# Kernel tuning notes

Hardware: AMD Instinct MI355X
Metric: run time of the kernel (lower is better)

Reference implementation:

```python
import jax, jax.numpy as jnp
import numpy as np

B = 32
HIST, C, H, W = 10, 11, 15, 20
D, NH, NL = 256, 4, 4
HD = D // NH
OUT, ADIM = 256, 20
L = HIST * H * W + 1  # 3001 tokens incl. cls
VIS = HIST * C * H * W  # 33000


def layernorm(x, g, b, eps=1e-5):
    m = jnp.mean(x, axis=-1, keepdims=True)
    v = jnp.mean((x - m) ** 2, axis=-1, keepdims=True)
    return (x - m) * jax.lax.rsqrt(v + eps) * g + b


def rope_1d(x):
    # x: [B, NH, L, HD]
    l, hd = x.shape[2], x.shape[3]
    t = jnp.arange(l, dtype=x.dtype)
    freqs = 10000.0 ** (-jnp.arange(0, hd, 2, dtype=x.dtype) / hd)
    emb = t[:, None] * freqs[None, :]            # [L, HD/2]
    emb = jnp.concatenate([emb, emb], axis=-1)   # [L, HD]
    cos = jnp.cos(emb)[None, None]
    sin = jnp.sin(emb)[None, None]
    x1, x2 = x[..., : hd // 2], x[..., hd // 2 :]
    rot = jnp.concatenate([-x2, x1], axis=-1)
    return x * cos + rot * sin


def lightning_attn(x, qw, kw, vw, ow, gq, bq, gk, bk):
    b, l, _ = x.shape
    q = layernorm(x @ qw, gq, bq)
    k = layernorm(x @ kw, gk, bk)
    v = x @ vw
    split = lambda a: a.reshape(b, l, NH, HD).transpose(0, 2, 1, 3)  # [B,NH,L,HD]
    q, k, v = split(q), split(k), split(v)
    q = jax.nn.silu(rope_1d(q))
    k = jax.nn.silu(rope_1d(k))
    kv = jnp.einsum('bhld,bhle->bhde', k, v)            # O(L) kv accumulation
    out = jnp.einsum('bhld,bhde->bhle', q, kv)
    out = out / jnp.sqrt(jnp.asarray(HD, x.dtype))
    out = out.transpose(0, 2, 1, 3).reshape(b, l, D)
    return out @ ow


def forward(obs_stack, proj_w, proj_b, cls_token, qw, kw, vw, ow, gq, bq, gk, bk,
            n1g, n1b, n2g, n2b, w1, b1, w2, b2, fng, fnb, out_w, out_b):
    b = obs_stack.shape[0]
    obs_feat = obs_stack[:, :VIS]
    action_feat = obs_stack[:, VIS:]
    vision = obs_feat.reshape(b, HIST, C, H, W).transpose(0, 1, 3, 4, 2)  # [B,T,H,W,C]
    x = vision @ proj_w + proj_b                                          # [B,T,H,W,D]
    x = x.reshape(b, -1, D)
    cls = jnp.broadcast_to(cls_token, (b, 1, D))
    x = jnp.concatenate([cls, x], axis=1)                                 # [B,L,D]
    for i in range(NL):
        h = lightning_attn(layernorm(x, n1g[i], n1b[i]), qw[i], kw[i], vw[i], ow[i],
                           gq[i], bq[i], gk[i], bk[i])
        x = x + h
        y = layernorm(x, n2g[i], n2b[i])
        y = jax.nn.gelu(y @ w1[i] + b1[i], approximate=False) @ w2[i] + b2[i]
        x = x + y
    x = layernorm(x, fng, fnb)
    cls_out = x[:, 0, :]
    final = jnp.concatenate([cls_out, action_feat], axis=1)
    return final @ out_w + out_b


def setup_inputs() -> dict:
    key = jax.random.key(0)
    ks = jax.random.split(key, 16)
    s = 0.02
    n = lambda k, shp: jax.random.normal(k, shp, dtype=jnp.float32) * s
    inp = {
        'obs_stack': jax.random.normal(ks[0], (B, VIS + ADIM), dtype=jnp.float32),
        'proj_w': n(ks[1], (C, D)),
        'proj_b': jnp.zeros((D,), jnp.float32),
        'cls_token': jax.random.normal(ks[2], (1, 1, D), dtype=jnp.float32),
        'qw': n(ks[3], (NL, D, D)),
        'kw': n(ks[4], (NL, D, D)),
        'vw': n(ks[5], (NL, D, D)),
        'ow': n(ks[6], (NL, D, D)),
        'gq': jnp.ones((NL, D), jnp.float32),
        'bq': jnp.zeros((NL, D), jnp.float32),
        'gk': jnp.ones((NL, D), jnp.float32),
        'bk': jnp.zeros((NL, D), jnp.float32),
        'n1g': jnp.ones((NL, D), jnp.float32),
        'n1b': jnp.zeros((NL, D), jnp.float32),
        'n2g': jnp.ones((NL, D), jnp.float32),
        'n2b': jnp.zeros((NL, D), jnp.float32),
        'w1': n(ks[7], (NL, D, 4 * D)),
        'b1': jnp.zeros((NL, 4 * D), jnp.float32),
        'w2': n(ks[8], (NL, 4 * D, D)),
        'b2': jnp.zeros((NL, D), jnp.float32),
        'fng': jnp.ones((D,), jnp.float32),
        'fnb': jnp.zeros((D,), jnp.float32),
        'out_w': n(ks[9], (D + ADIM, OUT)),
        'out_b': jnp.zeros((OUT,), jnp.float32),
    }
    return inp


def reference(obs_stack, proj_w, proj_b, cls_token, qw, kw, vw, ow, gq, bq, gk, bk,
              n1g, n1b, n2g, n2b, w1, b1, w2, b2, fng, fnb, out_w, out_b):
    return forward(obs_stack, proj_w, proj_b, cls_token, qw, kw, vw, ow, gq, bq, gk, bk,
                   n1g, n1b, n2g, n2b, w1, b1, w2, b2, fng, fnb, out_w, out_b)
```

## Files before the change

kernel.cpp:

```cpp
#include <hip/hip_runtime.h>
#include <math.h>

typedef unsigned short u16;
typedef __attribute__((ext_vector_type(8))) short short8;
typedef __attribute__((ext_vector_type(4))) short short4v;
typedef __attribute__((ext_vector_type(4))) float f32x4;

constexpr int B_    = 32;
constexpr int HIST_ = 10, C_ = 11, H_ = 15, W_ = 20;
constexpr int D_    = 256, NH_ = 4, NL_ = 4, HD_ = 64;
constexpr int OUT_  = 256, ADIM_ = 20;
constexpr int L_    = HIST_*H_*W_ + 1;
constexpr int VIS_  = HIST_*C_*H_*W_;
constexpr int NTOK  = B_*L_;
constexpr int OBSROW = VIS_ + ADIM_;
constexpr int PADR  = 128;

__device__ __forceinline__ float bf2f(u16 u) {
    return __uint_as_float(((unsigned)u) << 16);
}
__device__ __forceinline__ u16 f2bf(float f) {
    unsigned u = __float_as_uint(f);
    u = u + 0x7FFFu + ((u >> 16) & 1u);
    return (u16)(u >> 16);
}
__device__ __forceinline__ f32x4 mfma16(short8 a, short8 b, f32x4 c) {
    return __builtin_amdgcn_mfma_f32_16x16x32_bf16(a, b, c, 0, 0, 0);
}
__device__ __forceinline__ void gload16(const u16* gsrc, u16* ldsdst) {
    __builtin_amdgcn_global_load_lds(
        (const __attribute__((address_space(1))) unsigned int*)gsrc,
        (__attribute__((address_space(3))) unsigned int*)ldsdst,
        16, 0, 0);
}
__device__ __forceinline__ float gelu_fast(float v) {
    float t2 = 1.5957691216f*(v + 0.044715f*v*v*v);
    return v / (1.f + __expf(-t2));
}

__global__ void zero_kernel(float* __restrict__ p, int n) {
    int i = blockIdx.x*256 + threadIdx.x;
    if (i < n) p[i] = 0.f;
}

__global__ void wcvt_kernel(const float* __restrict__ src, u16* __restrict__ dst,
                            int Nn, int Kk, int dstLS, int dstOff) {
    int idx = blockIdx.x*256 + threadIdx.x;
    int tot = NL_*Nn*Kk;
    if (idx >= tot) return;
    int l = idx / (Nn*Kk);
    int rem = idx % (Nn*Kk);
    int n = rem / Kk, k = rem % Kk;
    dst[(size_t)l*dstLS + (size_t)(dstOff+n)*Kk + k] = f2bf(src[(size_t)l*Kk*Nn + (size_t)k*Nn + n]);
}

__global__ void rope_table_kernel(float* __restrict__ tab) {
    int idx = blockIdx.x*256 + threadIdx.x;
    if (idx >= L_*32) return;
    int t = idx >> 5, i = idx & 31;
    float freq = powf(10000.f, -2.f*(float)i/(float)HD_);
    float ang = (float)t * freq;
    tab[idx*2]   = cosf(ang);
    tab[idx*2+1] = sinf(ang);
}

__global__ __launch_bounds__(256) void proj_kernel(const float* __restrict__ obs,
        const float* __restrict__ pw, const float* __restrict__ pb,
        const float* __restrict__ cls, u16* __restrict__ x) {
    int wave = threadIdx.x >> 6, lane = threadIdx.x & 63;
    int n = blockIdx.x*4 + wave;
    if (n >= NTOK) return;
    int b = n / L_, l = n % L_;
    float4 acc;
    if (l == 0) {
        acc = ((const float4*)cls)[lane];
    } else {
        int t = l - 1;
        int hist = t / (H_*W_);
        int rem  = t % (H_*W_);
        float vv = 0.f;
        if (lane < C_) vv = obs[(size_t)b*OBSROW + hist*(C_*H_*W_) + lane*(H_*W_) + rem];
        acc = ((const float4*)pb)[lane];
        #pragma unroll
        for (int c = 0; c < C_; ++c) {
            float vc = __shfl(vv, c);
            float4 w4 = ((const float4*)(pw + c*D_))[lane];
            acc.x += vc*w4.x; acc.y += vc*w4.y; acc.z += vc*w4.z; acc.w += vc*w4.w;
        }
    }
    short4v o;
    o.x = (short)f2bf(acc.x); o.y = (short)f2bf(acc.y);
    o.z = (short)f2bf(acc.z); o.w = (short)f2bf(acc.w);
    *(short4v*)(x + (size_t)n*D_ + lane*4) = o;
}

__global__ __launch_bounds__(256) void ln_f2b_kernel(const u16* __restrict__ in,
        const float* __restrict__ g, const float* __restrict__ bt,
        u16* __restrict__ out, int ntok) {
    int wave = threadIdx.x >> 6, lane = threadIdx.x & 63;
    int n = blockIdx.x*4 + wave;
    if (n >= ntok) return;
    short4v raw = *(const short4v*)(in + (size_t)n*D_ + lane*4);
    float v0 = bf2f((u16)raw.x), v1 = bf2f((u16)raw.y), v2 = bf2f((u16)raw.z), v3 = bf2f((u16)raw.w);
    float s  = v0+v1+v2+v3;
    float sq = v0*v0+v1*v1+v2*v2+v3*v3;
    #pragma unroll
    for (int off = 32; off; off >>= 1) { s += __shfl_xor(s, off); sq += __shfl_xor(sq, off); }
    float mean = s * (1.f/D_);
    float var  = sq * (1.f/D_) - mean*mean;
    float r = rsqrtf(var + 1e-5f);
    float4 gg = ((const float4*)g)[lane];
    float4 bb = ((const float4*)bt)[lane];
    short4v o;
    o.x = (short)f2bf((v0-mean)*r*gg.x + bb.x);
    o.y = (short)f2bf((v1-mean)*r*gg.y + bb.y);
    o.z = (short)f2bf((v2-mean)*r*gg.z + bb.z);
    o.w = (short)f2bf((v3-mean)*r*gg.w + bb.w);
    *(short4v*)(out + (size_t)n*D_ + lane*4) = o;
}

template<int EPI, bool PB>
__global__ __launch_bounds__(256) void gemm_bf16(const u16* __restrict__ A, int lda,
        const u16* __restrict__ Wt, const float* __restrict__ bias,
        u16* __restrict__ Cb, u16* __restrict__ Xres, int M, int N, int K, int ldc) {
    __shared__ u16 As[2*128*32];
    __shared__ u16 Bs[2*128*32];
    const int gx = gridDim.x;
    int n = blockIdx.y * gx + blockIdx.x;
    const int nwg = gx * gridDim.y;
    if ((nwg & 7) == 0) n = (n & 7) * (nwg >> 3) + (n >> 3);
    const int bx = n % gx, by = n / gx;
    const int row0 = by*128, col0 = bx*128;

    size_t zrow = 0;
    if (PB) {
        int z = blockIdx.z;
        A  += (size_t)z * M * lda;
        Wt += (size_t)z * N * K;
        zrow = (size_t)z * M;
    }

    const int tid = threadIdx.x;
    const int wid = tid >> 6, lane = tid & 63;
    const int wr = wid >> 1, wc = wid & 1;

    f32x4 acc[4][4];
    #pragma unroll
    for (int i = 0; i < 4; ++i)
        #pragma unroll
        for (int j = 0; j < 4; ++j) {
            f32x4 z; z.x = 0.f; z.y = 0.f; z.z = 0.f; z.w = 0.f;
            acc[i][j] = z;
        }

    const int r0s = wid*32 + (lane>>2);
    const int r1s = r0s + 16;
    const int s0 = ((lane&3) - (r0s>>1)) & 3;
    const int s1 = ((lane&3) - (r1s>>1)) & 3;
    const u16* a0p = A  + (size_t)(row0 + r0s)*lda + s0*8;
    const u16* a1p = A  + (size_t)(row0 + r1s)*lda + s1*8;
    const u16* b0p = Wt + (size_t)(col0 + r0s)*K + s0*8;
    const u16* b1p = Wt + (size_t)(col0 + r1s)*K + s1*8;
    u16* lA0 = As + (wid*2+0)*512;
    u16* lA1 = As + (wid*2+1)*512;
    u16* lB0 = Bs + (wid*2+0)*512;
    u16* lB1 = Bs + (wid*2+1)*512;

    const int kg = lane >> 4, li = lane & 15;
    int aoff[4], boff[4];
    #pragma unroll
    for (int mi = 0; mi < 4; ++mi) {
        int row = wr*64 + mi*16 + li;
        aoff[mi] = row*32 + ((kg + (row>>1)) & 3)*8;
    }
    #pragma unroll
    for (int ni = 0; ni < 4; ++ni) {
        int row = wc*64 + ni*16 + li;
        boff[ni] = row*32 + ((kg + (row>>1)) & 3)*8;
    }

    auto stage = [&](int k0) {
        #pragma unroll
        for (int t = 0; t < 2; ++t) {
            const int ko = k0 + t*32;
            const int lo = t*4096;
            gload16(a0p + ko, lA0 + lo); gload16(a1p + ko, lA1 + lo);
            gload16(b0p + ko, lB0 + lo); gload16(b1p + ko, lB1 + lo);
        }
    };

    stage(0);
    const int nk2 = K >> 6;
    for (int ks = 0; ks < nk2; ++ks) {
        __syncthreads();
        short8 af[2][4], bfr[2][4];
        #pragma unroll
        for (int t = 0; t < 2; ++t) {
            #pragma unroll
            for (int mi = 0; mi < 4; ++mi) af[t][mi] = *(const short8*)(As + t*4096 + aoff[mi]);
            #pragma unroll
            for (int ni = 0; ni < 4; ++ni) bfr[t][ni] = *(const short8*)(Bs + t*4096 + boff[ni]);
        }
        __syncthreads();
        if (ks + 1 < nk2) stage((ks + 1) << 6);
        #pragma unroll
        for (int t = 0; t < 2; ++t)
            #pragma unroll
            for (int mi = 0; mi < 4; ++mi)
                #pragma unroll
                for (int ni = 0; ni < 4; ++ni)
                    acc[mi][ni] = mfma16(af[t][mi], bfr[t][ni], acc[mi][ni]);
    }

    #pragma unroll
    for (int mi = 0; mi < 4; ++mi) {
        int rbase = row0 + wr*64 + mi*16 + kg*4;
        #pragma unroll
        for (int ni = 0; ni < 4; ++ni) {
            int col = col0 + wc*64 + ni*16 + li;
            #pragma unroll
            for (int r = 0; r < 4; ++r) {
                int row = rbase + r;
                if (row >= M) continue;
                float v = acc[mi][ni][r];
                if (EPI == 1 || EPI == 3 || EPI == 4) v += bias[col];
                if (EPI == 1) v = gelu_fast(v);
                if (EPI == 2 || EPI == 3) {
                    size_t xi = (zrow + row)*(size_t)ldc + col;
                    Xres[xi] = f2bf(bf2f(Xres[xi]) + v);
                } else {
                    Cb[(zrow + row)*(size_t)ldc + col] = f2bf(v);
                }
            }
        }
    }
}

template<int EPI, bool PB>
__global__ __launch_bounds__(512) void gemm_wide(const u16* __restrict__ A, int lda,
        const u16* __restrict__ Wt, const float* __restrict__ bias,
        u16* __restrict__ Cb, int M, int N, int K, int ldc,
        const float* __restrict__ gqv = nullptr, const float* __restrict__ bqv = nullptr,
        const float* __restrict__ gkv = nullptr, const float* __restrict__ bkv = nullptr,
        const float* __restrict__ tab = nullptr) {
    __shared__ u16 As[2*4096];
    __shared__ u16 Bs[2*8192];
    const int gx = gridDim.x;
    int n = blockIdx.y * gx + blockIdx.x;
    const int nwg = gx * gridDim.y;
    if ((nwg & 7) == 0) n = (n & 7) * (nwg >> 3) + (n >> 3);
    const int bx = n % gx, by = n / gx;
    const int row0 = by*128, col0 = bx*256;

    size_t zrow = 0;
    if (PB) {
        int z = blockIdx.z;
        A  += (size_t)z * M * lda;
        Wt += (size_t)z * N * K;
        zrow = (size_t)z * M;
    }

    const int tid = threadIdx.x;
    const int wid = tid >> 6, lane = tid & 63;
    const int kg = lane >> 4, li = lane & 15;

    f32x4 acc[16];
    #pragma unroll
    for (int i = 0; i < 16; ++i) { f32x4 z; z.x=0.f; z.y=0.f; z.z=0.f; z.w=0.f; acc[i]=z; }

    const int ra = wid*16 + (lane>>2);
    const int sa = ((lane&3) - (ra>>1)) & 3;
    const u16* agp = A + (size_t)(row0 + ra)*lda + sa*8;
    const int lAo = wid*512;
    const int rb0 = (wid*2+0)*16 + (lane>>2);
    const int rb1 = (wid*2+1)*16 + (lane>>2);
    const int sb0 = ((lane&3) - (rb0>>1)) & 3;
    const int sb1 = ((lane&3) - (rb1>>1)) & 3;
    const u16* bgp0 = Wt + (size_t)(col0 + rb0)*K + sb0*8;
    const u16* bgp1 = Wt + (size_t)(col0 + rb1)*K + sb1*8;
    const int lB0o = (wid*2+0)*512;
    const int lB1o = (wid*2+1)*512;

    const int arow = wid*16 + li;
    const int aoff = arow*32 + ((kg + (arow>>1)) & 3)*8;
    int boff[16];
    #pragma unroll
    for (int ni = 0; ni < 16; ++ni) {
        int row = ni*16 + li;
        boff[ni] = row*32 + ((kg + (row>>1)) & 3)*8;
    }

    auto stage = [&](int k0) {
        #pragma unroll
        for (int t = 0; t < 2; ++t) {
            const int ko = k0 + t*32;
            gload16(agp  + ko, As + t*4096 + lAo);
            gload16(bgp0 + ko, Bs + t*8192 + lB0o);
            gload16(bgp1 + ko, Bs + t*8192 + lB1o);
        }
    };

    stage(0);
    const int nk2 = K >> 6;
    for (int ks = 0; ks < nk2; ++ks) {
        __syncthreads();
        short8 af0 = *(const short8*)(As + aoff);
        short8 b0[8], b1[8];
        #pragma unroll
        for (int ni = 0; ni < 8; ++ni) b0[ni] = *(const short8*)(Bs + boff[ni]);
        #pragma unroll
        for (int ni = 0; ni < 8; ++ni) acc[ni] = mfma16(af0, b0[ni], acc[ni]);
        #pragma unroll
        for (int ni = 0; ni < 8; ++ni) b1[ni] = *(const short8*)(Bs + boff[8+ni]);
        #pragma unroll
        for (int ni = 0; ni < 8; ++ni) acc[8+ni] = mfma16(af0, b1[ni], acc[8+ni]);
        short8 af1 = *(const short8*)(As + 4096 + aoff);
        #pragma unroll
        for (int ni = 0; ni < 8; ++ni) b0[ni] = *(const short8*)(Bs + 8192 + boff[ni]);
        #pragma unroll
        for (int ni = 0; ni < 8; ++ni) b1[ni] = *(const short8*)(Bs + 8192 + boff[8+ni]);
        __syncthreads();
        if (ks + 1 < nk2) stage((ks + 1) << 6);
        #pragma unroll
        for (int ni = 0; ni < 8; ++ni) acc[ni]   = mfma16(af1, b0[ni], acc[ni]);
        #pragma unroll
        for (int ni = 0; ni < 8; ++ni) acc[8+ni] = mfma16(af1, b1[ni], acc[8+ni]);
    }

    if constexpr (EPI == 2 || EPI == 3) {
        const bool doLN = (EPI == 2) ? (bx < 2) : (bx == 0);
        const float* g  = (EPI == 2) ? (bx ? gkv : gqv) : gkv;
        const float* bt = (EPI == 2) ? (bx ? bkv : bqv) : bkv;
        #pragma unroll
        for (int r = 0; r < 4; ++r) {
            const int row = row0 + wid*16 + kg*4 + r;
            const bool ok = row < M;
            if (doLN) {
                float o[16];
                float s = 0.f, sq = 0.f;
                #pragma unroll
                for (int ni = 0; ni < 16; ++ni) { float v = acc[ni][r]; o[ni] = v; s += v; sq += v*v; }
                s += __shfl_xor(s, 1); sq += __shfl_xor(sq, 1);
                s += __shfl_xor(s, 2); sq += __shfl_xor(sq, 2);
                s += __shfl_xor(s, 4); sq += __shfl_xor(sq, 4);
                s += __shfl_xor(s, 8); sq += __shfl_xor(sq, 8);
                float mean = s * (1.f/256.f);
                float var  = sq * (1.f/256.f) - mean*mean;
                float rstd = rsqrtf(var + 1e-5f);
                #pragma unroll
                for (int ni = 0; ni < 16; ++ni) {
                    int col = ni*16 + li;
                    o[ni] = (o[ni] - mean)*rstd*g[col] + bt[col];
                }
                if (ok) {
                    int l = row % L_;
                    #pragma unroll
                    for (int ni = 0; ni < 16; ++ni) {
                        int i32 = (ni&1)*16 + li;
                        float cs = tab[((size_t)l*32 + i32)*2];
                        float sn = tab[((size_t)l*32 + i32)*2 + 1];
                        float prt = o[ni^2];
                        float rv = ((ni&3) < 2) ? o[ni]*cs - prt*sn : o[ni]*cs + prt*sn;
                        rv = rv / (1.f + __expf(-rv));
                        Cb[(size_t)row*ldc + col0 + ni*16 + li] = f2bf(rv);
                    }
                }
            } else if (ok) {
                #pragma unroll
                for (int ni = 0; ni < 16; ++ni)
                    Cb[(size_t)row*ldc + col0 + ni*16 + li] = f2bf(acc[ni][r]);
            }
        }
        return;
    }

    #pragma unroll
    for (int r = 0; r < 4; ++r) {
        const int row = row0 + wid*16 + kg*4 + r;
        if (row >= M) continue;
        #pragma unroll
        for (int ni = 0; ni < 16; ++ni) {
            int col = col0 + ni*16 + li;
            float v = acc[ni][r];
            if (EPI == 1) { v += bias[col]; v = gelu_fast(v); }
            Cb[(zrow + row)*(size_t)ldc + col] = f2bf(v);
        }
    }
}

constexpr int KV_LSPLIT = 4;
constexpr int KV_PART   = 768;
__global__ __launch_bounds__(256) void kv_mfma_kernel(const u16* __restrict__ Kt,
        const u16* __restrict__ Vt, float* __restrict__ kvf, int ld) {
    __shared__ u16 kT[64][34];
    __shared__ u16 vT[64][34];
    const int bh = blockIdx.x;
    const int b = bh >> 2, h = bh & 3;
    const int tid = threadIdx.x;
    const int wid = tid >> 6, lane = tid & 63;
    const int kg = lane >> 4, li = lane & 15;
    const int wm = (wid >> 1)*32, wn = (wid & 1)*32;
    const int sl = tid >> 3;
    const int sd = (tid & 7) * 8;
    const u16* kbase = Kt + ((size_t)b*L_)*ld + h*HD_ + sd;
    const u16* vbase = Vt + ((size_t)b*L_)*ld + h*HD_ + sd;

    f32x4 acc[2][2];
    #pragma unroll
    for (int i = 0; i < 2; ++i)
        #pragma unroll
        for (int j = 0; j < 2; ++j) {
            f32x4 z; z.x=0.f; z.y=0.f; z.z=0.f; z.w=0.f; acc[i][j] = z;
        }

    const int l0p = blockIdx.y * KV_PART;
    for (int t = 0; t < KV_PART/32; ++t) {
        int gl = l0p + t*32 + sl;
        short8 kk = {0,0,0,0,0,0,0,0}, vv = {0,0,0,0,0,0,0,0};
        if (gl < L_) {
            kk = *(const short8*)(kbase + (size_t)gl*ld);
            vv = *(const short8*)(vbase + (size_t)gl*ld);
        }
        __syncthreads();
        #pragma unroll
        for (int j = 0; j < 8; ++j) {
            kT[sd+j][sl] = (u16)kk[j];
            vT[sd+j][sl] = (u16)vv[j];
        }
        __syncthreads();
        short8 a0, a1, b0, b1;
        {
            uint* d0 = (uint*)&a0; const uint* p0 = (const uint*)&kT[wm + li][kg*8];
            uint* d1 = (uint*)&a1; const uint* p1 = (const uint*)&kT[wm + 16 + li][kg*8];
            uint* d2 = (uint*)&b0; const uint* p2 = (const uint*)&vT[wn + li][kg*8];
            uint* d3 = (uint*)&b1; const uint* p3 = (const uint*)&vT[wn + 16 + li][kg*8];
            #pragma unroll
            for (int j = 0; j < 4; ++j) { d0[j]=p0[j]; d1[j]=p1[j]; d2[j]=p2[j]; d3[j]=p3[j]; }
        }
        acc[0][0] = mfma16(a0, b0, acc[0][0]);
        acc[0][1] = mfma16(a0, b1, acc[0][1]);
        acc[1][0] = mfma16(a1, b0, acc[1][0]);
        acc[1][1] = mfma16(a1, b1, acc[1][1]);
    }
    float* base = kvf + (size_t)bh*4096;
    #pragma unroll
    for (int mi = 0; mi < 2; ++mi)
        #pragma unroll
        for (int ni = 0; ni < 2; ++ni)
            #pragma unroll
            for (int r = 0; r < 4; ++r)
                atomicAdd(base + (wm + mi*16 + kg*4 + r)*64 + wn + ni*16 + li,
                          acc[mi][ni][r]);
}

__global__ __launch_bounds__(256) void m2_kernel(const float* __restrict__ kvf,
        const float* __restrict__ ow, u16* __restrict__ m2t) {
    __shared__ float kvs[64][64];
    const int bh = blockIdx.x;
    const int b = bh >> 2, h = bh & 3;
    const int tid = threadIdx.x;
    #pragma unroll
    for (int p = 0; p < 16; ++p)
        ((float*)kvs)[p*256 + tid] = kvf[(size_t)bh*4096 + p*256 + tid];
    __syncthreads();
    float acc[64];
    #pragma unroll
    for (int d = 0; d < 64; ++d) acc[d] = 0.f;
    for (int e = 0; e < 64; ++e) {
        float w = ow[(size_t)(h*64 + e)*256 + tid];
        #pragma unroll
        for (int d = 0; d < 64; ++d) acc[d] += kvs[d][e] * w;
    }
    u16* dst = m2t + ((size_t)b*256 + tid)*256 + h*64;
    #pragma unroll
    for (int d = 0; d < 64; ++d) dst[d] = f2bf(acc[d]*0.125f);
}

__global__ __launch_bounds__(256) void tail_kernel(const u16* __restrict__ Xn,
        const u16* __restrict__ qwT,
        const float* __restrict__ gqv, const float* __restrict__ bqv,
        const u16* __restrict__ m2t, u16* __restrict__ x,
        const float* __restrict__ g2, const float* __restrict__ bt2,
        const u16* __restrict__ w1T, const float* __restrict__ b1v,
        const u16* __restrict__ w2T, const float* __restrict__ b2v) {
    __shared__ float xn0[256];
    __shared__ float qrow[256];
    __shared__ float y[256];
    __shared__ float h[1024];
    __shared__ float red[8];
    const int bl = blockIdx.x;
    const int tid = threadIdx.x;
    const int wave = tid >> 6, lane = tid & 63;
    const size_t row = (size_t)bl * L_;
    xn0[tid] = bf2f(Xn[row*256 + tid]);
    __syncthreads();
    {
        const u16* qwrow = qwT + (size_t)tid*256;
        float qa = 0.f;
        for (int k = 0; k < 256; k += 8) {
            short8 w = *(const short8*)(qwrow + k);
            qa += xn0[k+0]*bf2f((u16)w[0]) + xn0[k+1]*bf2f((u16)w[1])
                + xn0[k+2]*bf2f((u16)w[2]) + xn0[k+3]*bf2f((u16)w[3])
                + xn0[k+4]*bf2f((u16)w[4]) + xn0[k+5]*bf2f((u16)w[5])
                + xn0[k+6]*bf2f((u16)w[6]) + xn0[k+7]*bf2f((u16)w[7]);
        }
        float s = qa, sq = qa*qa;
        #pragma unroll
        for (int off = 32; off; off >>= 1) { s += __shfl_xor(s, off); sq += __shfl_xor(sq, off); }
        if (lane == 0) { red[wave] = s; red[4+wave] = sq; }
        __syncthreads();
        s  = red[0]+red[1]+red[2]+red[3];
        sq = red[4]+red[5]+red[6]+red[7];
        float mean = s*(1.f/256.f), var = sq*(1.f/256.f) - mean*mean;
        float rstd = rsqrtf(var + 1e-5f);
        float qn = (qa - mean)*rstd*gqv[tid] + bqv[tid];
        qrow[tid] = qn / (1.f + __expf(-qn));
    }
    __syncthreads();
    const u16* mrow = m2t + ((size_t)bl*256 + tid)*256;
    float acc = 0.f;
    for (int d = 0; d < 256; d += 8) {
        short8 w = *(const short8*)(mrow + d);
        acc += qrow[d+0]*bf2f((u16)w[0]) + qrow[d+1]*bf2f((u16)w[1])
             + qrow[d+2]*bf2f((u16)w[2]) + qrow[d+3]*bf2f((u16)w[3])
             + qrow[d+4]*bf2f((u16)w[4]) + qrow[d+5]*bf2f((u16)w[5])
             + qrow[d+6]*bf2f((u16)w[6]) + qrow[d+7]*bf2f((u16)w[7]);
    }
    float v = bf2f(x[row*256 + tid]) + acc;
    float s = v, sq = v*v;
    #pragma unroll
    for (int off = 32; off; off >>= 1) { s += __shfl_xor(s, off); sq += __shfl_xor(sq, off); }
    if (lane == 0) { red[wave] = s; red[4+wave] = sq; }
    __syncthreads();
    s  = red[0]+red[1]+red[2]+red[3];
    sq = red[4]+red[5]+red[6]+red[7];
    float mean = s*(1.f/256.f), var = sq*(1.f/256.f) - mean*mean;
    float rstd = rsqrtf(var + 1e-5f);
    y[tid] = (v - mean)*rstd*g2[tid] + bt2[tid];
    __syncthreads();
    #pragma unroll
    for (int jj = 0; jj < 4; ++jj) {
        int j = tid*4 + jj;
        const u16* wrow = w1T + (size_t)j*256;
        float a = b1v[j];
        for (int k = 0; k < 256; k += 8) {
            short8 w = *(const short8*)(wrow + k);
            a += y[k+0]*bf2f((u16)w[0]) + y[k+1]*bf2f((u16)w[1])
               + y[k+2]*bf2f((u16)w[2]) + y[k+3]*bf2f((u16)w[3])
               + y[k+4]*bf2f((u16)w[4]) + y[k+5]*bf2f((u16)w[5])
               + y[k+6]*bf2f((u16)w[6]) + y[k+7]*bf2f((u16)w[7]);
        }
        h[j] = gelu_fast(a);
    }
    __syncthreads();
    const u16* w2row = w2T + (size_t)tid*1024;
    float a2 = b2v[tid];
    for (int k = 0; k < 1024; k += 8) {
        short8 w = *(const short8*)(w2row + k);
        a2 += h[k+0]*bf2f((u16)w[0]) + h[k+1]*bf2f((u16)w[1])
            + h[k+2]*bf2f((u16)w[2]) + h[k+3]*bf2f((u16)w[3])
            + h[k+4]*bf2f((u16)w[4]) + h[k+5]*bf2f((u16)w[5])
            + h[k+6]*bf2f((u16)w[6]) + h[k+7]*bf2f((u16)w[7]);
    }
    x[row*256 + tid] = f2bf(v + a2);
}

__global__ void head_kernel(const u16* __restrict__ x, const float* __restrict__ obs,
                            const float* __restrict__ fng, const float* __restrict__ fnb,
                            const float* __restrict__ ow, const float* __restrict__ ob,
                            float* __restrict__ out) {
    __shared__ float row[D_ + ADIM_];
    __shared__ float red[8];
    int b = blockIdx.x, tid = threadIdx.x;
    float v = bf2f(x[((size_t)b*L_)*D_ + tid]);
    float s = v, sq = v*v;
    #pragma unroll
    for (int off = 32; off; off >>= 1) { s += __shfl_xor(s, off); sq += __shfl_xor(sq, off); }
    int wave = tid >> 6, lane = tid & 63;
    if (lane == 0) { red[wave] = s; red[4+wave] = sq; }
    __syncthreads();
    s  = red[0]+red[1]+red[2]+red[3];
    sq = red[4]+red[5]+red[6]+red[7];
    float mean = s*(1.f/D_), var = sq*(1.f/D_) - mean*mean;
    float r = rsqrtf(var + 1e-5f);
    row[tid] = (v-mean)*r*fng[tid] + fnb[tid];
    if (tid < ADIM_) row[D_+tid] = obs[(size_t)b*OBSROW + VIS_ + tid];
    __syncthreads();
    float acc = ob[tid];
    for (int j = 0; j < D_+ADIM_; ++j) acc += row[j]*ow[j*OUT_ + tid];
    out[(size_t)b*OUT_ + tid] = acc;
}

extern "C" void kernel_launch(void* const* d_in, const int* in_sizes, int n_in,
                              void* d_out, int out_size, void* d_ws, size_t ws_size,
                              hipStream_t stream) {
    const float* obs   = (const float*)d_in[0];
    const float* pw    = (const float*)d_in[1];
    const float* pb    = (const float*)d_in[2];
    const float* cls   = (const float*)d_in[3];
    const float* qw    = (const float*)d_in[4];
    const float* kw    = (const float*)d_in[5];
    const float* vw    = (const float*)d_in[6];
    const float* oww   = (const float*)d_in[7];
    const float* gq    = (const float*)d_in[8];
    const float* bq    = (const float*)d_in[9];
    const float* gk    = (const float*)d_in[10];
    const float* bk    = (const float*)d_in[11];
    const float* n1g   = (const float*)d_in[12];
    const float* n1b   = (const float*)d_in[13];
    const float* n2g   = (const float*)d_in[14];
    const float* n2b   = (const float*)d_in[15];
    const float* w1    = (const float*)d_in[16];
    const float* b1    = (const float*)d_in[17];
    const float* w2    = (const float*)d_in[18];
    const float* b2    = (const float*)d_in[19];
    const float* fng   = (const float*)d_in[20];
    const float* fnb   = (const float*)d_in[21];
    const float* outw  = (const float*)d_in[22];
    const float* outb  = (const float*)d_in[23];

    u16* x    = (u16*)d_ws;
    u16* qkvT = x + (size_t)NTOK*D_;
    u16* w1T  = qkvT + (size_t)NL_*768*256;
    u16* w2T  = w1T  + (size_t)NL_*262144;
    float* tab = (float*)(w2T + (size_t)NL_*262144);
    float* kvf_all = tab + (size_t)L_*32*2;
    u16* bufs = (u16*)(kvf_all + (size_t)NL_*B_*NH_*4096);

    size_t fixedB = (size_t)((char*)bufs - (char*)d_ws);
    auto needed = [&](int nb) -> size_t {
        size_t t = (size_t)nb * L_;
        return fixedB + (t*256 + (size_t)PADR*256)*2 + (t*1024 + (size_t)PADR*1024)*2
               + (size_t)nb*65536*2;
    };
    int nbc = 32;
    while (nbc > 1 && needed(nbc) > ws_size) nbc >>= 1;
    const int nch = B_ / nbc;
    const int RCn = nbc * L_;

    u16* Xn   = bufs;
    u16* QKVc = Xn + (size_t)RCn*256 + (size_t)PADR*256;
    u16* Hc   = QKVc;
    u16* M2T  = QKVc + (size_t)RCn*1024 + (size_t)PADR*1024;

    wcvt_kernel<<<(NL_*65536 + 255)/256, 256, 0, stream>>>(qw,  qkvT, 256, 256, 768*256, 0);
    wcvt_kernel<<<(NL_*65536 + 255)/256, 256, 0, stream>>>(kw,  qkvT, 256, 256, 768*256, 256);
    wcvt_kernel<<<(NL_*65536 + 255)/256, 256, 0, stream>>>(vw,  qkvT, 256, 256, 768*256, 512);
    wcvt_kernel<<<(NL_*262144 + 255)/256, 256, 0, stream>>>(w1, w1T, 1024, 256, 262144, 0);
    wcvt_kernel<<<(NL_*262144 + 255)/256, 256, 0, stream>>>(w2, w2T, 256, 1024, 262144, 0);
    rope_table_kernel<<<(L_*32 + 255)/256, 256, 0, stream>>>(tab);
    zero_kernel<<<(NL_*B_*NH_*4096 + 255)/256, 256, 0, stream>>>(kvf_all, NL_*B_*NH_*4096);
    proj_kernel<<<(NTOK + 3)/4, 256, 0, stream>>>(obs, pw, pb, cls, x);

    const int gy  = (RCn + 127)/128;
    const int lnb = (RCn + 3)/4;
    const int nbh = nbc*NH_;

    for (int c = 0; c < nch; ++c) {
        u16* xc = x + (size_t)c*RCn*D_;
        ln_f2b_kernel<<<lnb, 256, 0, stream>>>(xc, n1g, n1b, Xn, RCn);

        for (int layer = 0; layer < NL_; ++layer) {
            const u16* qkvT_l = qkvT + (size_t)layer*768*256;
            const u16* w1T_l  = w1T  + (size_t)layer*262144;
            const u16* w2T_l  = w2T  + (size_t)layer*262144;
            const float* ow_l = oww + (size_t)layer*65536;
            const float* b1_l = b1 + (size_t)layer*1024;
            const float* b2_l = b2 + (size_t)layer*D_;
            float* kvf = kvf_all + ((size_t)(c*NL_ + layer))*nbh*4096;

            if (layer < NL_-1) {
                gemm_wide<2,false><<<dim3(3, gy), 512, 0, stream>>>(Xn, 256, qkvT_l, nullptr,
                        QKVc, RCn, 768, 256, 768,
                        gq + layer*D_, bq + layer*D_, gk + layer*D_, bk + layer*D_, tab);
            } else {
                gemm_wide<3,false><<<dim3(2, gy), 512, 0, stream>>>(Xn, 256, qkvT_l + 65536, nullptr,
                        QKVc + 256, RCn, 512, 256, 768,
                        nullptr, nullptr, gk + layer*D_, bk + layer*D_, tab);
            }
            kv_mfma_kernel<<<dim3(nbh, KV_LSPLIT), 256, 0, stream>>>(QKVc + 256, QKVc + 512, kvf, 768);
            m2_kernel<<<nbh, 256, 0, stream>>>(kvf, ow_l, M2T);

            if (layer < NL_-1) {
                gemm_bf16<2,true><<<dim3(2, 24, nbc), 256, 0, stream>>>(QKVc, 768, M2T, nullptr, nullptr, xc, L_, 256, 256, 256);
                ln_f2b_kernel<<<lnb, 256, 0, stream>>>(xc, n2g + layer*D_, n2b + layer*D_, Xn, RCn);
                gemm_wide<1,false><<<dim3(4, gy), 512, 0, stream>>>(Xn, 256, w1T_l, b1_l, Hc, RCn, 1024, 256, 1024);
                gemm_bf16<3,false><<<dim3(2, gy), 256, 0, stream>>>(Hc, 1024, w2T_l, b2_l, nullptr, xc, RCn, 256, 1024, 256);
                ln_f2b_kernel<<<lnb, 256, 0, stream>>>(xc, n1g + (layer+1)*D_, n1b + (layer+1)*D_, Xn, RCn);
            } else {
                tail_kernel<<<nbc, 256, 0, stream>>>(Xn, qkvT_l, gq + layer*D_, bq + layer*D_,
                                                     M2T, xc, n2g + layer*D_, n2b + layer*D_,
                                                     w1T_l, b1_l, w2T_l, b2_l);
            }
        }
    }

    head_kernel<<<B_, 256, 0, stream>>>(x, obs, fng, fnb, outw, outb, (float*)d_out);
}
```

Baseline: 2.129 ms.

## Fuse residual add and LayerNorm into wide GEMM epilogues for out-proj and FFN2

Replaces the 128x128 gemm_bf16 plus separate ln_f2b kernel with a 128x256 gemm_wide variant whose tile covers the full 256-wide row. The epilogue adds the residual, writes it back, and computes the row LayerNorm via lane shuffles. This removes two LayerNorm launches per layer and their re-read of the residual stream. In exchange the grid has half as many blocks, which may reduce occupancy on these N=256 GEMMs.

```diff
diff --git a/kernel.cpp b/kernel.cpp
--- a/kernel.cpp
+++ b/kernel.cpp
@@ -120,129 +120,12 @@
 }
 
 template<int EPI, bool PB>
-__global__ __launch_bounds__(256) void gemm_bf16(const u16* __restrict__ A, int lda,
-        const u16* __restrict__ Wt, const float* __restrict__ bias,
-        u16* __restrict__ Cb, u16* __restrict__ Xres, int M, int N, int K, int ldc) {
-    __shared__ u16 As[2*128*32];
-    __shared__ u16 Bs[2*128*32];
-    const int gx = gridDim.x;
-    int n = blockIdx.y * gx + blockIdx.x;
-    const int nwg = gx * gridDim.y;
-    if ((nwg & 7) == 0) n = (n & 7) * (nwg >> 3) + (n >> 3);
-    const int bx = n % gx, by = n / gx;
-    const int row0 = by*128, col0 = bx*128;
-
-    size_t zrow = 0;
-    if (PB) {
-        int z = blockIdx.z;
-        A  += (size_t)z * M * lda;
-        Wt += (size_t)z * N * K;
-        zrow = (size_t)z * M;
-    }
-
-    const int tid = threadIdx.x;
-    const int wid = tid >> 6, lane = tid & 63;
-    const int wr = wid >> 1, wc = wid & 1;
-
-    f32x4 acc[4][4];
-    #pragma unroll
-    for (int i = 0; i < 4; ++i)
-        #pragma unroll
-        for (int j = 0; j < 4; ++j) {
-            f32x4 z; z.x = 0.f; z.y = 0.f; z.z = 0.f; z.w = 0.f;
-            acc[i][j] = z;
-        }
-
-    const int r0s = wid*32 + (lane>>2);
-    const int r1s = r0s + 16;
-    const int s0 = ((lane&3) - (r0s>>1)) & 3;
-    const int s1 = ((lane&3) - (r1s>>1)) & 3;
-    const u16* a0p = A  + (size_t)(row0 + r0s)*lda + s0*8;
-    const u16* a1p = A  + (size_t)(row0 + r1s)*lda + s1*8;
-    const u16* b0p = Wt + (size_t)(col0 + r0s)*K + s0*8;
-    const u16* b1p = Wt + (size_t)(col0 + r1s)*K + s1*8;
-    u16* lA0 = As + (wid*2+0)*512;
-    u16* lA1 = As + (wid*2+1)*512;
-    u16* lB0 = Bs + (wid*2+0)*512;
-    u16* lB1 = Bs + (wid*2+1)*512;
-
-    const int kg = lane >> 4, li = lane & 15;
-    int aoff[4], boff[4];
-    #pragma unroll
-    for (int mi = 0; mi < 4; ++mi) {
-        int row = wr*64 + mi*16 + li;
-        aoff[mi] = row*32 + ((kg + (row>>1)) & 3)*8;
-    }
-    #pragma unroll
-    for (int ni = 0; ni < 4; ++ni) {
-        int row = wc*64 + ni*16 + li;
-        boff[ni] = row*32 + ((kg + (row>>1)) & 3)*8;
-    }
-
-    auto stage = [&](int k0) {
-        #pragma unroll
-        for (int t = 0; t < 2; ++t) {
-            const int ko = k0 + t*32;
-            const int lo = t*4096;
-            gload16(a0p + ko, lA0 + lo); gload16(a1p + ko, lA1 + lo);
-            gload16(b0p + ko, lB0 + lo); gload16(b1p + ko, lB1 + lo);
-        }
-    };
-
-    stage(0);
-    const int nk2 = K >> 6;
-    for (int ks = 0; ks < nk2; ++ks) {
-        __syncthreads();
-        short8 af[2][4], bfr[2][4];
-        #pragma unroll
-        for (int t = 0; t < 2; ++t) {
-            #pragma unroll
-            for (int mi = 0; mi < 4; ++mi) af[t][mi] = *(const short8*)(As + t*4096 + aoff[mi]);
-            #pragma unroll
-            for (int ni = 0; ni < 4; ++ni) bfr[t][ni] = *(const short8*)(Bs + t*4096 + boff[ni]);
-        }
-        __syncthreads();
-        if (ks + 1 < nk2) stage((ks + 1) << 6);
-        #pragma unroll
-        for (int t = 0; t < 2; ++t)
-            #pragma unroll
-            for (int mi = 0; mi < 4; ++mi)
-                #pragma unroll
-                for (int ni = 0; ni < 4; ++ni)
-                    acc[mi][ni] = mfma16(af[t][mi], bfr[t][ni], acc[mi][ni]);
-    }
-
-    #pragma unroll
-    for (int mi = 0; mi < 4; ++mi) {
-        int rbase = row0 + wr*64 + mi*16 + kg*4;
-        #pragma unroll
-        for (int ni = 0; ni < 4; ++ni) {
-            int col = col0 + wc*64 + ni*16 + li;
-            #pragma unroll
-            for (int r = 0; r < 4; ++r) {
-                int row = rbase + r;
-                if (row >= M) continue;
-                float v = acc[mi][ni][r];
-                if (EPI == 1 || EPI == 3 || EPI == 4) v += bias[col];
-                if (EPI == 1) v = gelu_fast(v);
-                if (EPI == 2 || EPI == 3) {
-                    size_t xi = (zrow + row)*(size_t)ldc + col;
-                    Xres[xi] = f2bf(bf2f(Xres[xi]) + v);
-                } else {
-                    Cb[(zrow + row)*(size_t)ldc + col] = f2bf(v);
-                }
-            }
-        }
-    }
-}
-
-template<int EPI, bool PB>
 __global__ __launch_bounds__(512) void gemm_wide(const u16* __restrict__ A, int lda,
         const u16* __restrict__ Wt, const float* __restrict__ bias,
         u16* __restrict__ Cb, int M, int N, int K, int ldc,
         const float* __restrict__ gqv = nullptr, const float* __restrict__ bqv = nullptr,
         const float* __restrict__ gkv = nullptr, const float* __restrict__ bkv = nullptr,
-        const float* __restrict__ tab = nullptr) {
+        const float* __restrict__ tab = nullptr, u16* __restrict__ Xres = nullptr) {
     __shared__ u16 As[2*4096];
     __shared__ u16 Bs[2*8192];
     const int gx = gridDim.x;
@@ -374,6 +257,48 @@
         return;
     }
 
+    if constexpr (EPI == 4 || EPI == 5) {
+        #pragma unroll
+        for (int r = 0; r < 4; ++r) {
+            const int row = row0 + wid*16 + kg*4 + r;
+            const bool ok = row < M;
+            float o[16];
+            #pragma unroll
+            for (int ni = 0; ni < 16; ++ni) {
+                float v = acc[ni][r];
+                if (EPI == 5) v += bias[ni*16 + li];
+                o[ni] = v;
+            }
+            if (ok) {
+                #pragma unroll
+                for (int ni = 0; ni < 16; ++ni) {
+                    size_t xi = (zrow + row)*(size_t)ldc + ni*16 + li;
+                    float nv = o[ni] + bf2f(Xres[xi]);
+                    Xres[xi] = f2bf(nv);
+                    o[ni] = nv;
+                }
+            }
+            float s = 0.f, sq = 0.f;
+            #pragma unroll
+            for (int ni = 0; ni < 16; ++ni) { s += o[ni]; sq += o[ni]*o[ni]; }
+            s += __shfl_xor(s, 1); sq += __shfl_xor(sq, 1);
+            s += __shfl_xor(s, 2); sq += __shfl_xor(sq, 2);
+            s += __shfl_xor(s, 4); sq += __shfl_xor(sq, 4);
+            s += __shfl_xor(s, 8); sq += __shfl_xor(sq, 8);
+            float mean = s * (1.f/256.f);
+            float var  = sq * (1.f/256.f) - mean*mean;
+            float rstd = rsqrtf(var + 1e-5f);
+            if (ok) {
+                #pragma unroll
+                for (int ni = 0; ni < 16; ++ni) {
+                    int col = ni*16 + li;
+                    Cb[(zrow + row)*(size_t)ldc + col] = f2bf((o[ni]-mean)*rstd*gqv[col] + bqv[col]);
+                }
+            }
+        }
+        return;
+    }
+
     #pragma unroll
     for (int r = 0; r < 4; ++r) {
         const int row = row0 + wid*16 + kg*4 + r;
@@ -682,11 +607,13 @@
             m2_kernel<<<nbh, 256, 0, stream>>>(kvf, ow_l, M2T);
 
             if (layer < NL_-1) {
-                gemm_bf16<2,true><<<dim3(2, 24, nbc), 256, 0, stream>>>(QKVc, 768, M2T, nullptr, nullptr, xc, L_, 256, 256, 256);
-                ln_f2b_kernel<<<lnb, 256, 0, stream>>>(xc, n2g + layer*D_, n2b + layer*D_, Xn, RCn);
+                gemm_wide<4,true><<<dim3(1, 24, nbc), 512, 0, stream>>>(QKVc, 768, M2T, nullptr,
+                        Xn, L_, 256, 256, 256,
+                        n2g + layer*D_, n2b + layer*D_, nullptr, nullptr, nullptr, xc);
                 gemm_wide<1,false><<<dim3(4, gy), 512, 0, stream>>>(Xn, 256, w1T_l, b1_l, Hc, RCn, 1024, 256, 1024);
-                gemm_bf16<3,false><<<dim3(2, gy), 256, 0, stream>>>(Hc, 1024, w2T_l, b2_l, nullptr, xc, RCn, 256, 1024, 256);
-                ln_f2b_kernel<<<lnb, 256, 0, stream>>>(xc, n1g + (layer+1)*D_, n1b + (layer+1)*D_, Xn, RCn);
+                gemm_wide<5,false><<<dim3(1, gy), 512, 0, stream>>>(Hc, 1024, w2T_l, b2_l,
+                        Xn, RCn, 256, 1024, 256,
+                        n1g + (layer+1)*D_, n1b + (layer+1)*D_, nullptr, nullptr, nullptr, xc);
             } else {
                 tail_kernel<<<nbc, 256, 0, stream>>>(Xn, qkvT_l, gq + layer*D_, bq + layer*D_,
                                                      M2T, xc, n2g + layer*D_, n2b + layer*D_,
```

Result: no change. 2.159 ms (+1.4%).
